# Performance work log

Hardware: AMD Instinct MI355X
Metric: run time of the kernel (lower is better)

The kernel has to match this reference:

```python
import jax, jax.numpy as jnp
import numpy as np

B, T, HID = 2, 2048, 2048
N_HEADS, N_KV, HEAD_DIM = 32, 8, 64
THETA = 10000.0
SCALE = HEAD_DIM ** -0.5
STEPS = 2  # entries already in cache before this call (step_idx)


def _rope_cos_sin(pos):
    # pos: [B, T] int -> cos/sin [B, T, HEAD_DIM]
    inv_freq = 1.0 / (THETA ** (jnp.arange(0, HEAD_DIM, 2, dtype=jnp.float32) / HEAD_DIM))
    freqs = pos.astype(jnp.float32)[..., None] * inv_freq  # [B,T,D/2]
    emb = jnp.concatenate([freqs, freqs], axis=-1)
    return jnp.cos(emb), jnp.sin(emb)


def _rotate_half(x):
    x1, x2 = jnp.split(x, 2, axis=-1)
    return jnp.concatenate([-x2, x1], axis=-1)


def setup_inputs() -> dict:
    key = jax.random.key(0)
    ks = jax.random.split(key, 8)
    combined_states = jax.random.normal(ks[0], (B, T, 2 * HID), dtype=jnp.float32)
    # additive causal mask: 0 on/below diagonal, large negative above
    causal = jnp.tril(jnp.ones((T, T), dtype=bool))
    attention_mask = jnp.where(causal, 0.0, -1e9).astype(jnp.float32)[None, None].repeat(B, axis=0)
    position_ids = jnp.broadcast_to(jnp.arange(T, dtype=jnp.int32), (B, T))
    prev_k = jax.random.normal(ks[1], (STEPS, B, N_HEADS, T, HEAD_DIM), dtype=jnp.float32)
    prev_v = jax.random.normal(ks[2], (STEPS, B, N_HEADS, T, HEAD_DIM), dtype=jnp.float32)
    Wq = 0.02 * jax.random.normal(ks[3], (2 * HID, N_HEADS * HEAD_DIM), dtype=jnp.float32)
    Wk = 0.02 * jax.random.normal(ks[4], (2 * HID, N_KV * HEAD_DIM), dtype=jnp.float32)
    Wv = 0.02 * jax.random.normal(ks[5], (2 * HID, N_KV * HEAD_DIM), dtype=jnp.float32)
    Wo = 0.02 * jax.random.normal(ks[6], (N_HEADS * HEAD_DIM, HID), dtype=jnp.float32)
    return {"combined_states": combined_states, "attention_mask": attention_mask,
            "position_ids": position_ids, "prev_k": prev_k, "prev_v": prev_v,
            "Wq": Wq, "Wk": Wk, "Wv": Wv, "Wo": Wo}


def reference(combined_states, attention_mask, position_ids, prev_k, prev_v, Wq, Wk, Wv, Wo):
    b, t, _ = combined_states.shape
    step_idx = prev_k.shape[0]  # len(cache_k) before append
    groups = N_HEADS // N_KV

    # fused QKV projection -> [B, H, T, D]
    q = (combined_states @ Wq).reshape(b, t, N_HEADS, HEAD_DIM).transpose(0, 2, 1, 3)
    k = (combined_states @ Wk).reshape(b, t, N_KV, HEAD_DIM).transpose(0, 2, 1, 3)
    v = (combined_states @ Wv).reshape(b, t, N_KV, HEAD_DIM).transpose(0, 2, 1, 3)

    # RoPE with phase shift by step_idx
    cos, sin = _rope_cos_sin(position_ids + step_idx)
    cos, sin = cos[:, None], sin[:, None]  # [B,1,T,D]
    q = q * cos + _rotate_half(q) * sin
    k = k * cos + _rotate_half(k) * sin

    # GQA expansion (repeat_interleave over head dim)
    k = jnp.repeat(k, groups, axis=1)
    v = jnp.repeat(v, groups, axis=1)

    # cache after append: [prev_0, prev_1, ..., k_new]; k0 = cache[0], later = cache[1:]
    k0, v0 = prev_k[0], prev_v[0]
    later_k = jnp.concatenate([prev_k[1:], k[None]], axis=0)  # [S, B, H, T, D], S = step_idx
    later_v = jnp.concatenate([prev_v[1:], v[None]], axis=0)

    # block attention over K_0 plus growing diagonal terms
    attn = jnp.einsum('bhtd,bhsd->bhts', q, k0) * SCALE + attention_mask  # [B,H,T,T]
    diag = jnp.einsum('bhtd,sbhtd->bhts', q, later_k) * SCALE             # [B,H,T,S]
    logits = jnp.concatenate([attn, diag], axis=-1)                        # [B,H,T,T+S]
    probs = jax.nn.softmax(logits.astype(jnp.float32), axis=-1).astype(q.dtype)

    out = jnp.einsum('bhts,bhsd->bhtd', probs[..., :t], v0)
    out = out + jnp.einsum('bhts,sbhtd->bhtd', probs[..., t:], later_v)
    out = out.transpose(0, 2, 1, 3).reshape(b, t, N_HEADS * HEAD_DIM)
    return out @ Wo
```

## Files before the change

### kernel.cpp

```cpp
#include <hip/hip_runtime.h>

#define B_    2
#define T_    2048
#define HID_  2048
#define NH_   32
#define NKV_  8
#define HD_   64
#define STEPS_ 2
#define SCALE_ 0.125f
#define CSC_  0.18033688011112042f

typedef float   f32x4  __attribute__((ext_vector_type(4)));
typedef __bf16  bf16x8 __attribute__((ext_vector_type(8)));
typedef unsigned short u16x8 __attribute__((ext_vector_type(8)));

__device__ __forceinline__ unsigned short f2bf(float f) {
  unsigned int u = __builtin_bit_cast(unsigned int, f);
  u = (u + 0x7fffu + ((u >> 16) & 1u)) >> 16;
  return (unsigned short)u;
}
__device__ __forceinline__ float bf2f(unsigned short h) {
  unsigned int u = ((unsigned int)h) << 16;
  return __builtin_bit_cast(float, u);
}
__device__ __forceinline__ bf16x8 frag_ld(const unsigned short* p) {
  u16x8 v = *(const u16x8*)p;
  return __builtin_bit_cast(bf16x8, v);
}
__device__ __forceinline__ f32x4 mfma16(bf16x8 a, bf16x8 b, f32x4 c) {
  return __builtin_amdgcn_mfma_f32_16x16x32_bf16(a, b, c, 0, 0, 0);
}
__device__ __forceinline__ void async_cp16(const void* g, void* l) {
  __builtin_amdgcn_global_load_lds(
      (const __attribute__((address_space(1))) void*)g,
      (__attribute__((address_space(3))) void*)l, 16, 0, 0);
}
__device__ __forceinline__ unsigned int cvtpk_bf16(float lo, float hi) {
  unsigned int r;
  asm("v_cvt_pk_bf16_f32 %0, %1, %2" : "=v"(r) : "v"(lo), "v"(hi));
  return r;
}

__global__ __launch_bounds__(256) void convert_bf16(const float* __restrict__ in,
                                                    unsigned short* __restrict__ out,
                                                    int n4) {
  int idx = blockIdx.x * 256 + threadIdx.x;
  if (idx < n4) {
    float4 v = ((const float4*)in)[idx];
    ushort4 o;
    o.x = f2bf(v.x); o.y = f2bf(v.y); o.z = f2bf(v.z); o.w = f2bf(v.w);
    ((ushort4*)out)[idx] = o;
  }
}

__global__ __launch_bounds__(256) void transpose_f32_bf16_ld(const float* __restrict__ in,
                                                             unsigned short* __restrict__ out,
                                                             int K, int N, int ldo) {
  __shared__ float tile[64][65];
  int n0 = blockIdx.x * 64, k0 = blockIdx.y * 64;
  int c = threadIdx.x & 63, w = threadIdx.x >> 6;
#pragma unroll
  for (int i = 0; i < 16; i++) {
    int r = w * 16 + i;
    tile[r][c] = in[(size_t)(k0 + r) * N + n0 + c];
  }
  __syncthreads();
#pragma unroll
  for (int i = 0; i < 16; i++) {
    int rr = w * 16 + i;
    out[(size_t)(n0 + rr) * ldo + k0 + c] = f2bf(tile[c][rr]);
  }
}

__global__ __launch_bounds__(256) void transpose_v0(const float* __restrict__ v0,
                                                    unsigned short* __restrict__ v0t) {
  __shared__ float tile[64][65];
  int s0 = blockIdx.x * 64;
  int bh = blockIdx.y;
  const float* src = v0 + (size_t)bh * T_ * HD_;
  unsigned short* dst = v0t + (size_t)bh * HD_ * T_;
  int c = threadIdx.x & 63, w = threadIdx.x >> 6;
#pragma unroll
  for (int i = 0; i < 16; i++) {
    int r = w * 16 + i;
    tile[r][c] = src[(size_t)(s0 + r) * HD_ + c];
  }
  __syncthreads();
#pragma unroll
  for (int i = 0; i < 16; i++) {
    int rr = w * 16 + i;
    dst[(size_t)rr * T_ + s0 + c] = f2bf(tile[c][rr]);
  }
}

#define SBAR  do { __builtin_amdgcn_sched_barrier(0); __builtin_amdgcn_s_barrier(); \
                   __builtin_amdgcn_sched_barrier(0); } while (0)
#define LGKM0 do { asm volatile("s_waitcnt lgkmcnt(0)" ::: "memory"); \
                   __builtin_amdgcn_sched_barrier(0); } while (0)
#define VM2   do { asm volatile("s_waitcnt vmcnt(2)" ::: "memory"); } while (0)
#define VM0   do { asm volatile("s_waitcnt vmcnt(0)" ::: "memory"); } while (0)

template <int NF>
__global__ __launch_bounds__(512, 2) void gemm128_bt(const unsigned short* __restrict__ A,
                                                     const unsigned short* __restrict__ Bt,
                                                     float* __restrict__ C,
                                                     int M, int N, int K) {
  constexpr int NHF = NF / 2;
  constexpr int BROWS = 128 + NF * 64;
  __shared__ __attribute__((aligned(128))) unsigned short smem[2][BROWS * 64];

  const int tid  = threadIdx.x;
  const int lane = tid & 63;
  const int wid  = tid >> 6;
  const int wr   = wid >> 2;
  const int wc   = wid & 3;
  const int la   = lane & 15;
  const int lq   = lane >> 4;
  const int sw   = la & 7;
  const int m0   = blockIdx.x * 128;
  const int n0   = blockIdx.y * (NF * 64);

  const int sr = lane >> 3;
  const int sl = (lane & 7) ^ sr;

  const unsigned short* gA[2];
  const unsigned short* gB[NHF][2];
#pragma unroll
  for (int is = 0; is < 2; ++is) {
    int r = (wid * 2 + is) * 8 + sr;
    gA[is] = A + (size_t)(m0 + r) * K + sl * 8;
#pragma unroll
    for (int u = 0; u < NHF; ++u)
      gB[u][is] = Bt + (size_t)(n0 + u * 128 + r) * K + sl * 8;
  }

#define G_STG_A(buf, kt) do { \
    async_cp16(gA[0] + (size_t)(kt) * 64, &smem[buf][(wid * 2 + 0) * 512]); \
    async_cp16(gA[1] + (size_t)(kt) * 64, &smem[buf][(wid * 2 + 1) * 512]); \
  } while (0)
#define G_STG_B(buf, u, kt) do { \
    async_cp16(gB[u][0] + (size_t)(kt) * 64, &smem[buf][(128 + (u) * 128) * 64 + (wid * 2 + 0) * 512]); \
    async_cp16(gB[u][1] + (size_t)(kt) * 64, &smem[buf][(128 + (u) * 128) * 64 + (wid * 2 + 1) * 512]); \
  } while (0)

  f32x4  acc[4][NF] = {};
  bf16x8 aR[2][2], b0r[NHF][2], b1r[NHF][2];

#define G_RD_A(buf, qm) do { \
    const unsigned short* rp_ = &smem[buf][0]; \
    _Pragma("unroll") \
    for (int i_ = 0; i_ < 2; ++i_) { \
      int ro_ = (wr * 64 + (qm) * 32 + i_ * 16 + la) * 64; \
      aR[i_][0] = frag_ld(rp_ + ro_ + (((0 + lq) ^ sw) << 3)); \
      aR[i_][1] = frag_ld(rp_ + ro_ + (((4 + lq) ^ sw) << 3)); \
    } \
  } while (0)
#define G_RD_B(buf, qn, breg) do { \
    const unsigned short* rp_ = &smem[buf][128 * 64]; \
    _Pragma("unroll") \
    for (int j_ = 0; j_ < NHF; ++j_) { \
      int ro_ = (wc * (NF * 16) + (qn) * (NF * 8) + j_ * 16 + la) * 64; \
      breg[j_][0] = frag_ld(rp_ + ro_ + (((0 + lq) ^ sw) << 3)); \
      breg[j_][1] = frag_ld(rp_ + ro_ + (((4 + lq) ^ sw) << 3)); \
    } \
  } while (0)
#define G_MMA(qm, qn, breg) do { \
    _Pragma("unroll") \
    for (int i_ = 0; i_ < 2; ++i_) \
      _Pragma("unroll") \
      for (int j_ = 0; j_ < NHF; ++j_) { \
        f32x4 c_ = acc[(qm) * 2 + i_][(qn) * NHF + j_]; \
        c_ = mfma16(aR[i_][0], breg[j_][0], c_); \
        c_ = mfma16(aR[i_][1], breg[j_][1], c_); \
        acc[(qm) * 2 + i_][(qn) * NHF + j_] = c_; \
      } \
  } while (0)

  G_STG_A(0, 0);
#pragma unroll
  for (int u = 0; u < NHF; ++u) G_STG_B(0, u, 0);
  if constexpr (NF == 6) G_STG_B(1, 2, 1); else G_STG_A(1, 1);
  VM2;
  SBAR;

  const int NI = K >> 7;
  for (int it = 0; it < NI; ++it) {
    const int e = it * 2;
    const bool pf = (it + 1 < NI);
    G_RD_A(0, 0);
    G_RD_B(0, 0, b0r);
    if constexpr (NF == 6) G_STG_A(1, e + 1); else G_STG_B(1, 0, e + 1);
    SBAR; LGKM0;
    __builtin_amdgcn_s_setprio(1); G_MMA(0, 0, b0r); __builtin_amdgcn_s_setprio(0);
    SBAR;
    G_RD_B(0, 1, b1r);
    if constexpr (NF == 6) G_STG_B(1, 0, e + 1); else G_STG_B(1, 1, e + 1);
    SBAR; LGKM0;
    __builtin_amdgcn_s_setprio(1); G_MMA(0, 1, b1r); __builtin_amdgcn_s_setprio(0);
    SBAR;
    G_RD_A(0, 1);
    if constexpr (NF == 6) G_STG_B(1, 1, e + 1);
    SBAR; LGKM0;
    __builtin_amdgcn_s_setprio(1); G_MMA(1, 1, b1r); __builtin_amdgcn_s_setprio(0);
    SBAR;
    if (pf) G_STG_A(0, e + 2);
    SBAR; LGKM0;
    __builtin_amdgcn_s_setprio(1); G_MMA(1, 0, b0r); __builtin_amdgcn_s_setprio(0);
    if (pf) { VM2; } else { VM0; }
    SBAR;
    G_RD_A(1, 0);
    G_RD_B(1, 0, b0r);
    if (pf) G_STG_B(0, 0, e + 2);
    SBAR; LGKM0;
    __builtin_amdgcn_s_setprio(1); G_MMA(0, 0, b0r); __builtin_amdgcn_s_setprio(0);
    SBAR;
    G_RD_B(1, 1, b1r);
    if (pf) G_STG_B(0, 1, e + 2);
    SBAR; LGKM0;
    __builtin_amdgcn_s_setprio(1); G_MMA(0, 1, b1r); __builtin_amdgcn_s_setprio(0);
    SBAR;
    G_RD_A(1, 1);
    if constexpr (NF == 6) { if (pf) G_STG_B(0, 2, e + 2); }
    SBAR; LGKM0;
    __builtin_amdgcn_s_setprio(1); G_MMA(1, 1, b1r); __builtin_amdgcn_s_setprio(0);
    SBAR;
    if constexpr (NF == 6) { if (pf) G_STG_B(1, 2, e + 3); }
    else                   { if (pf) G_STG_A(1, e + 3); }
    SBAR; LGKM0;
    __builtin_amdgcn_s_setprio(1); G_MMA(1, 0, b0r); __builtin_amdgcn_s_setprio(0);
    VM2;
    SBAR;
  }

#pragma unroll
  for (int mf = 0; mf < 4; ++mf) {
    int row = m0 + wr * 64 + mf * 16 + lq * 4;
#pragma unroll
    for (int nf = 0; nf < NF; ++nf) {
      int col = n0 + wc * (NF * 16) + nf * 16 + la;
#pragma unroll
      for (int r = 0; r < 4; ++r)
        C[(size_t)(row + r) * N + col] = acc[mf][nf][r];
    }
  }
#undef G_STG_A
#undef G_STG_B
#undef G_RD_A
#undef G_RD_B
#undef G_MMA
}

__global__ __launch_bounds__(256) void rope_kernel(const float* __restrict__ QKV,
                                                   const int* __restrict__ pos_ids,
                                                   unsigned short* __restrict__ q_b,
                                                   float* __restrict__ knew) {
  int idx = blockIdx.x * 256 + threadIdx.x;
  const int total = B_ * T_ * (NH_ + NKV_) * 32;
  if (idx >= total) return;
  int i = idx & 31;
  int tmp = idx >> 5;
  int hh = tmp % (NH_ + NKV_);
  int bt = tmp / (NH_ + NKV_);
  int t = bt & (T_ - 1);
  int b = bt >> 11;
  int pos = pos_ids[bt] + STEPS_;
  float inv = exp2f(-(float)i * (13.287712379549449f / 32.0f));
  float ang = (float)pos * inv;
  float sn, cs;
  sincosf(ang, &sn, &cs);
  const float* rowp = QKV + (size_t)bt * 3072;
  if (hh < NH_) {
    float x1 = rowp[hh * 64 + i];
    float x2 = rowp[hh * 64 + 32 + i];
    float y1 = (x1 * cs - x2 * sn) * CSC_;
    float y2 = (x2 * cs + x1 * sn) * CSC_;
    size_t o = ((size_t)(b * NH_ + hh) * T_ + t) * HD_ + i;
    q_b[o] = f2bf(y1);
    q_b[o + 32] = f2bf(y2);
  } else {
    int kv = hh - NH_;
    float x1 = rowp[2048 + kv * 64 + i];
    float x2 = rowp[2048 + kv * 64 + 32 + i];
    float y1 = x1 * cs - x2 * sn;
    float y2 = x2 * cs + x1 * sn;
    size_t o = ((size_t)(b * NKV_ + kv) * T_ + t) * HD_ + i;
    knew[o] = y1;
    knew[o + 32] = y2;
  }
}

__global__ __launch_bounds__(256, 3) void flash_kernel(const unsigned short* __restrict__ qb,
                                                       const unsigned short* __restrict__ k0b,
                                                       const unsigned short* __restrict__ v0t,
                                                       float* __restrict__ Of,
                                                       float* __restrict__ ml) {
  __shared__ unsigned short sK[2][64 * 64];
  __shared__ unsigned short sV[2][64 * 64];
  __shared__ unsigned short sP[4][16 * 72];

  const int tid = threadIdx.x;
  const int lane = tid & 63;
  const int wave = tid >> 6;
  const int la = lane & 15;
  const int lq = lane >> 4;
  const int swz = la & 7;

  const int id = blockIdx.x;
  const int bh = (id & 7) * 8 + ((id >> 3) & 7);
  const int qt = 15 - (id >> 6);

  const size_t bhs = (size_t)bh;
  const unsigned short* gK = k0b + bhs * T_ * HD_;
  const unsigned short* gV = v0t + bhs * HD_ * T_;

  const int rb0 = qt * 128 + wave * 32;
  const int ktd = rb0 >> 6;
  const int ktmax = 2 * qt + 1;

  bf16x8 aq[2][2];
#pragma unroll
  for (int f = 0; f < 2; f++) {
    const unsigned short* qp = qb + (bhs * T_ + rb0 + f * 16 + la) * HD_;
    aq[f][0] = frag_ld(qp + lq * 8);
    aq[f][1] = frag_ld(qp + 32 + lq * 8);
  }

  f32x4 o[2][4] = {};
  float m_f[2] = {-1e30f, -1e30f};
  float l_f[2] = {0.0f, 0.0f};

  const int lrow = lane >> 3;
  const int lcb = (lane & 7) ^ lrow;

  {
    unsigned short* kd = &sK[0][wave * 1024];
    unsigned short* vd = &sV[0][wave * 1024];
    async_cp16(gK + (size_t)(wave * 16 + lrow) * HD_ + lcb * 8, kd);
    async_cp16(gK + (size_t)(wave * 16 + 8 + lrow) * HD_ + lcb * 8, kd + 512);
    async_cp16(gV + (size_t)(wave * 16 + lrow) * T_ + lcb * 8, vd);
    async_cp16(gV + (size_t)(wave * 16 + 8 + lrow) * T_ + lcb * 8, vd + 512);
  }
  __syncthreads();

  int cur = 0;
  for (int kt = 0; kt <= ktmax; ++kt) {
    if (kt < ktmax) {
      const int nk = (kt + 1) * 64;
      unsigned short* kd = &sK[cur ^ 1][wave * 1024];
      unsigned short* vd = &sV[cur ^ 1][wave * 1024];
      async_cp16(gK + (size_t)(nk + wave * 16 + lrow) * HD_ + lcb * 8, kd);
      async_cp16(gK + (size_t)(nk + wave * 16 + 8 + lrow) * HD_ + lcb * 8, kd + 512);
      async_cp16(gV + (size_t)(wave * 16 + lrow) * T_ + nk + lcb * 8, vd);
      async_cp16(gV + (size_t)(wave * 16 + 8 + lrow) * T_ + nk + lcb * 8, vd + 512);
    }

    if (kt <= ktd) {
      const unsigned short* kb = &sK[cur][0];
      const unsigned short* vb = &sV[cur][0];

      bf16x8 bk0[4], bk1[4];
#pragma unroll
      for (int nb = 0; nb < 4; nb++) {
        const unsigned short* rp = kb + (nb * 16 + la) * 64;
        bk0[nb] = frag_ld(rp + ((lq ^ swz) << 3));
        bk1[nb] = frag_ld(rp + (((lq + 4) ^ swz) << 3));
      }
      f32x4 s[2][4];
      __builtin_amdgcn_s_setprio(1);
#pragma unroll
      for (int f = 0; f < 2; f++)
#pragma unroll
        for (int nb = 0; nb < 4; nb++) {
          f32x4 z = {0.f, 0.f, 0.f, 0.f};
          z = mfma16(bk0[nb], aq[f][0], z);
          z = mfma16(bk1[nb], aq[f][1], z);
          s[f][nb] = z;
        }
      __builtin_amdgcn_s_setprio(0);

      const bool diag = (kt == ktd);
#pragma unroll
      for (int f = 0; f < 2; f++) {
        const int qrow = rb0 + f * 16 + la;
        if (diag) {
#pragma unroll
          for (int nb = 0; nb < 4; nb++)
#pragma unroll
            for (int r = 0; r < 4; r++) {
              int key = kt * 64 + nb * 16 + lq * 4 + r;
              s[f][nb][r] = (key <= qrow) ? s[f][nb][r] : -1e30f;
            }
        }
        float t0 = fmaxf(fmaxf(s[f][0][0], s[f][0][1]), fmaxf(s[f][0][2], s[f][0][3]));
        float t1 = fmaxf(fmaxf(s[f][1][0], s[f][1][1]), fmaxf(s[f][1][2], s[f][1][3]));
        float t2 = fmaxf(fmaxf(s[f][2][0], s[f][2][1]), fmaxf(s[f][2][2], s[f][2][3]));
        float t3 = fmaxf(fmaxf(s[f][3][0], s[f][3][1]), fmaxf(s[f][3][2], s[f][3][3]));
        float tm = fmaxf(fmaxf(t0, t1), fmaxf(t2, t3));
        tm = fmaxf(tm, __shfl_xor(tm, 16));
        tm = fmaxf(tm, __shfl_xor(tm, 32));
        const bool resc = __any(tm > m_f[f] + 8.0f);
        if (resc) {
          float mn = fmaxf(m_f[f], tm);
          float al = exp2f(m_f[f] - mn);
          m_f[f] = mn;
          l_f[f] *= al;
          float a0 = __shfl(al, lq * 4 + 0);
          float a1 = __shfl(al, lq * 4 + 1);
          float a2 = __shfl(al, lq * 4 + 2);
          float a3 = __shfl(al, lq * 4 + 3);
#pragma unroll
          for (int jd = 0; jd < 4; jd++) {
            o[f][jd][0] *= a0;
            o[f][jd][1] *= a1;
            o[f][jd][2] *= a2;
            o[f][jd][3] *= a3;
          }
        }
        float ls = 0.0f;
#pragma unroll
        for (int nb = 0; nb < 4; nb++)
#pragma unroll
          for (int r = 0; r < 4; r++) {
            float p = exp2f(s[f][nb][r] - m_f[f]);
            s[f][nb][r] = p;
            ls += p;
          }
        ls += __shfl_xor(ls, 16);
        ls += __shfl_xor(ls, 32);
        l_f[f] += ls;
      }

      bf16x8 bv0[4], bv1[4];
#pragma unroll
      for (int jd = 0; jd < 4; jd++) {
        const unsigned short* rp = vb + (jd * 16 + la) * 64;
        bv0[jd] = frag_ld(rp + ((lq ^ swz) << 3));
        bv1[jd] = frag_ld(rp + (((lq + 4) ^ swz) << 3));
      }
      unsigned short* pw = &sP[wave][0];
#pragma unroll
      for (int f = 0; f < 2; f++) {
#pragma unroll
        for (int nb = 0; nb < 4; nb++) {
          unsigned int p01 = cvtpk_bf16(s[f][nb][0], s[f][nb][1]);
          unsigned int p23 = cvtpk_bf16(s[f][nb][2], s[f][nb][3]);
          unsigned long long pq = ((unsigned long long)p23 << 32) | (unsigned long long)p01;
          *(unsigned long long*)(pw + la * 72 + nb * 16 + lq * 4) = pq;
        }
        bf16x8 ap0 = frag_ld(&pw[la * 72 + lq * 8]);
        bf16x8 ap1 = frag_ld(&pw[la * 72 + 32 + lq * 8]);
        __builtin_amdgcn_s_setprio(1);
#pragma unroll
        for (int jd = 0; jd < 4; jd++) {
          o[f][jd] = mfma16(ap0, bv0[jd], o[f][jd]);
          o[f][jd] = mfma16(ap1, bv1[jd], o[f][jd]);
        }
        __builtin_amdgcn_s_setprio(0);
      }
    }
    __syncthreads();
    cur ^= 1;
  }

#pragma unroll
  for (int f = 0; f < 2; f++)
#pragma unroll
    for (int jd = 0; jd < 4; jd++)
#pragma unroll
      for (int r = 0; r < 4; r++) {
        int row = rb0 + f * 16 + lq * 4 + r;
        Of[(bhs * T_ + row) * HD_ + jd * 16 + la] = o[f][jd][r];
      }
  if (lq == 0) {
#pragma unroll
    for (int f = 0; f < 2; f++) {
      int row = rb0 + f * 16 + la;
      ml[(bhs * T_ + row) * 2] = m_f[f];
      ml[(bhs * T_ + row) * 2 + 1] = l_f[f];
    }
  }
}

__global__ __launch_bounds__(256) void attn_epilogue(const unsigned short* __restrict__ qb,
                                                     const float* __restrict__ prev_k,
                                                     const float* __restrict__ prev_v,
                                                     const float* __restrict__ knew,
                                                     const float* __restrict__ QKV,
                                                     const float* __restrict__ Of,
                                                     const float* __restrict__ ml,
                                                     unsigned short* __restrict__ attnout) {
  const int lane = threadIdx.x & 63;
  const int wave = threadIdx.x >> 6;
  const int row = blockIdx.x * 4 + wave;
  const int b = row >> 16;
  const int h = (row >> 11) & 31;
  const int t = row & 2047;
  const int d = lane;
  const size_t base = (size_t)row * HD_ + d;

  float q = bf2f(qb[base]);
  const size_t p1i = ((size_t)B_ * NH_ * T_ * HD_) + (((size_t)b * NH_ + h) * T_ + t) * HD_ + d;
  float k1 = prev_k[p1i];
  float v1 = prev_v[p1i];
  int kv = h >> 2;
  float kn = knew[(((size_t)b * NKV_ + kv) * T_ + t) * HD_ + d];
  float vn = QKV[((size_t)(b * T_ + t)) * 3072 + 2560 + kv * 64 + d];

  float e1 = q * k1, e2 = q * kn;
#pragma unroll
  for (int off = 1; off < 64; off <<= 1) {
    e1 += __shfl_xor(e1, off);
    e2 += __shfl_xor(e2, off);
  }

  float m = ml[(size_t)row * 2];
  float l = ml[(size_t)row * 2 + 1];
  float mf = fmaxf(m, fmaxf(e1, e2));
  float w0 = exp2f(m - mf), w1 = exp2f(e1 - mf), w2 = exp2f(e2 - mf);
  float denom = l * w0 + w1 + w2;
  float out = (Of[base] * w0 + v1 * w1 + vn * w2) / denom;

  attnout[((size_t)(b * T_ + t)) * (NH_ * HD_) + h * HD_ + d] = f2bf(out);
}

#define OFF_QKV   ((size_t)0)
#define OFF_XB    ((size_t)50331648)
#define OFF_WQKVT ((size_t)83886080)
#define OFF_WOT   ((size_t)109051904)
#define OFF_QB    ((size_t)117440512)
#define OFF_K0B   ((size_t)134217728)
#define OFF_V0T   ((size_t)150994944)
#define OFF_KNEW  ((size_t)167772160)
#define OFF_ML    ((size_t)176160768)

extern "C" void kernel_launch(void* const* d_in, const int* in_sizes, int n_in,
                              void* d_out, int out_size, void* d_ws, size_t ws_size,
                              hipStream_t stream) {
  const float* X = (const float*)d_in[0];
  const int* pos = (const int*)d_in[2];
  const float* prevk = (const float*)d_in[3];
  const float* prevv = (const float*)d_in[4];
  const float* Wq = (const float*)d_in[5];
  const float* Wk = (const float*)d_in[6];
  const float* Wv = (const float*)d_in[7];
  const float* Wo = (const float*)d_in[8];

  char* ws = (char*)d_ws;
  float* QKV = (float*)(ws + OFF_QKV);
  unsigned short* Xb = (unsigned short*)(ws + OFF_XB);
  float* Of = (float*)(ws + OFF_XB);
  unsigned short* WqkvT = (unsigned short*)(ws + OFF_WQKVT);
  unsigned short* attnout = (unsigned short*)(ws + OFF_WQKVT);
  unsigned short* WoT = (unsigned short*)(ws + OFF_WOT);
  unsigned short* q_b = (unsigned short*)(ws + OFF_QB);
  unsigned short* k0b = (unsigned short*)(ws + OFF_K0B);
  unsigned short* v0t = (unsigned short*)(ws + OFF_V0T);
  float* knew = (float*)(ws + OFF_KNEW);
  float* ml = (float*)(ws + OFF_ML);

  convert_bf16<<<16384, 256, 0, stream>>>(X, Xb, 4194304);
  transpose_f32_bf16_ld<<<dim3(32, 64), 256, 0, stream>>>(Wq, WqkvT, 4096, 2048, 4096);
  transpose_f32_bf16_ld<<<dim3(8, 64), 256, 0, stream>>>(Wk, WqkvT + (size_t)2048 * 4096, 4096, 512, 4096);
  transpose_f32_bf16_ld<<<dim3(8, 64), 256, 0, stream>>>(Wv, WqkvT + (size_t)2560 * 4096, 4096, 512, 4096);
  transpose_f32_bf16_ld<<<dim3(32, 32), 256, 0, stream>>>(Wo, WoT, 2048, 2048, 2048);
  convert_bf16<<<8192, 256, 0, stream>>>(prevk, k0b, 2097152);
  transpose_v0<<<dim3(32, 64), 256, 0, stream>>>(prevv, v0t);

  gemm128_bt<6><<<dim3(32, 8), 512, 0, stream>>>(Xb, WqkvT, QKV, 4096, 3072, 4096);

  rope_kernel<<<20480, 256, 0, stream>>>(QKV, pos, q_b, knew);

  flash_kernel<<<1024, 256, 0, stream>>>(q_b, k0b, v0t, Of, ml);

  attn_epilogue<<<32768, 256, 0, stream>>>(q_b, prevk, prevv, knew, QKV, Of, ml, attnout);

  gemm128_bt<4><<<dim3(32, 8), 512, 0, stream>>>(attnout, WoT, (float*)d_out, 4096, 2048, 2048);
}
```

Measured before the change: 523.1 us.

## Fuse diagonal-term epilogue into flash attention kernel, drop O/ml round trip

The separate attention epilogue kernel is removed and its work moves into the end of the flash kernel. Each block now computes the two extra diagonal logits from its register-resident Q fragments and combines them with its running max and sum. It then writes the normalized bf16 output directly. This removes the fp32 O and m/l intermediate writes and reads plus one kernel launch, but the fused tail does strided, poorly coalesced global loads of prev_k/prev_v/knew/QKV inside a kernel with occupancy pressure.

```diff
diff --git a/kernel.cpp b/kernel.cpp
--- a/kernel.cpp
+++ b/kernel.cpp
@@ -292,8 +292,11 @@
 __global__ __launch_bounds__(256, 3) void flash_kernel(const unsigned short* __restrict__ qb,
                                                        const unsigned short* __restrict__ k0b,
                                                        const unsigned short* __restrict__ v0t,
-                                                       float* __restrict__ Of,
-                                                       float* __restrict__ ml) {
+                                                       const float* __restrict__ prev_k,
+                                                       const float* __restrict__ prev_v,
+                                                       const float* __restrict__ knew,
+                                                       const float* __restrict__ QKV,
+                                                       unsigned short* __restrict__ attnout) {
   __shared__ unsigned short sK[2][64 * 64];
   __shared__ unsigned short sV[2][64 * 64];
   __shared__ unsigned short sP[4][16 * 72];
@@ -462,65 +465,61 @@
     cur ^= 1;
   }
 
-#pragma unroll
-  for (int f = 0; f < 2; f++)
-#pragma unroll
-    for (int jd = 0; jd < 4; jd++)
-#pragma unroll
-      for (int r = 0; r < 4; r++) {
-        int row = rb0 + f * 16 + lq * 4 + r;
-        Of[(bhs * T_ + row) * HD_ + jd * 16 + la] = o[f][jd][r];
+  const int bI = bh >> 5;
+  const int hI = bh & 31;
+  const int kvI = hI >> 2;
+  const size_t P1 = (size_t)B_ * NH_ * T_ * HD_;
+  const float* k1base = prev_k + P1 + bhs * T_ * HD_;
+  const float* v1base = prev_v + P1 + bhs * T_ * HD_;
+  const float* knbase = knew + ((size_t)bI * NKV_ + kvI) * T_ * HD_;
+  const float* vnbase = QKV + (size_t)bI * T_ * 3072 + 2560 + kvI * 64;
+  unsigned short* aobase = attnout + (size_t)bI * T_ * (NH_ * HD_) + hI * HD_;
+
+#pragma unroll
+  for (int f = 0; f < 2; f++) {
+    const int rowA = rb0 + f * 16 + la;
+    const float* k1p = k1base + (size_t)rowA * HD_;
+    const float* knp = knbase + (size_t)rowA * HD_;
+    float e1 = 0.f, e2 = 0.f;
+#pragma unroll
+    for (int h2 = 0; h2 < 2; h2++) {
+      const int dd = h2 * 32 + lq * 8;
+#pragma unroll
+      for (int j = 0; j < 8; j++) {
+        float qv = (float)aq[f][h2][j];
+        e1 = fmaf(qv, k1p[dd + j], e1);
+        e2 = fmaf(qv, knp[dd + j], e2);
       }
-  if (lq == 0) {
-#pragma unroll
-    for (int f = 0; f < 2; f++) {
-      int row = rb0 + f * 16 + la;
-      ml[(bhs * T_ + row) * 2] = m_f[f];
-      ml[(bhs * T_ + row) * 2 + 1] = l_f[f];
     }
-  }
-}
-
-__global__ __launch_bounds__(256) void attn_epilogue(const unsigned short* __restrict__ qb,
-                                                     const float* __restrict__ prev_k,
-                                                     const float* __restrict__ prev_v,
-                                                     const float* __restrict__ knew,
-                                                     const float* __restrict__ QKV,
-                                                     const float* __restrict__ Of,
-                                                     const float* __restrict__ ml,
-                                                     unsigned short* __restrict__ attnout) {
-  const int lane = threadIdx.x & 63;
-  const int wave = threadIdx.x >> 6;
-  const int row = blockIdx.x * 4 + wave;
-  const int b = row >> 16;
-  const int h = (row >> 11) & 31;
-  const int t = row & 2047;
-  const int d = lane;
-  const size_t base = (size_t)row * HD_ + d;
-
-  float q = bf2f(qb[base]);
-  const size_t p1i = ((size_t)B_ * NH_ * T_ * HD_) + (((size_t)b * NH_ + h) * T_ + t) * HD_ + d;
-  float k1 = prev_k[p1i];
-  float v1 = prev_v[p1i];
-  int kv = h >> 2;
-  float kn = knew[(((size_t)b * NKV_ + kv) * T_ + t) * HD_ + d];
-  float vn = QKV[((size_t)(b * T_ + t)) * 3072 + 2560 + kv * 64 + d];
-
-  float e1 = q * k1, e2 = q * kn;
-#pragma unroll
-  for (int off = 1; off < 64; off <<= 1) {
-    e1 += __shfl_xor(e1, off);
-    e2 += __shfl_xor(e2, off);
-  }
-
-  float m = ml[(size_t)row * 2];
-  float l = ml[(size_t)row * 2 + 1];
-  float mf = fmaxf(m, fmaxf(e1, e2));
-  float w0 = exp2f(m - mf), w1 = exp2f(e1 - mf), w2 = exp2f(e2 - mf);
-  float denom = l * w0 + w1 + w2;
-  float out = (Of[base] * w0 + v1 * w1 + vn * w2) / denom;
-
-  attnout[((size_t)(b * T_ + t)) * (NH_ * HD_) + h * HD_ + d] = f2bf(out);
+    e1 += __shfl_xor(e1, 16); e1 += __shfl_xor(e1, 32);
+    e2 += __shfl_xor(e2, 16); e2 += __shfl_xor(e2, 32);
+    float mx = fmaxf(m_f[f], fmaxf(e1, e2));
+    float w0 = exp2f(m_f[f] - mx);
+    float w1 = exp2f(e1 - mx);
+    float w2 = exp2f(e2 - mx);
+    float inv = 1.0f / (l_f[f] * w0 + w1 + w2);
+    float s0 = w0 * inv, s1 = w1 * inv, s2 = w2 * inv;
+    float a0[4], a1[4], a2[4];
+#pragma unroll
+    for (int r = 0; r < 4; r++) {
+      a0[r] = __shfl(s0, lq * 4 + r);
+      a1[r] = __shfl(s1, lq * 4 + r);
+      a2[r] = __shfl(s2, lq * 4 + r);
+    }
+#pragma unroll
+    for (int r = 0; r < 4; r++) {
+      const int rowO = rb0 + f * 16 + lq * 4 + r;
+      const float* v1p = v1base + (size_t)rowO * HD_;
+      const float* vnp = vnbase + (size_t)rowO * 3072;
+      unsigned short* aop = aobase + (size_t)rowO * (NH_ * HD_);
+#pragma unroll
+      for (int jd = 0; jd < 4; jd++) {
+        int d = jd * 16 + la;
+        float out = o[f][jd][r] * a0[r] + v1p[d] * a1[r] + vnp[d] * a2[r];
+        aop[d] = f2bf(out);
+      }
+    }
+  }
 }
 
 #define OFF_QKV   ((size_t)0)
@@ -548,7 +547,6 @@
   char* ws = (char*)d_ws;
   float* QKV = (float*)(ws + OFF_QKV);
   unsigned short* Xb = (unsigned short*)(ws + OFF_XB);
-  float* Of = (float*)(ws + OFF_XB);
   unsigned short* WqkvT = (unsigned short*)(ws + OFF_WQKVT);
   unsigned short* attnout = (unsigned short*)(ws + OFF_WQKVT);
   unsigned short* WoT = (unsigned short*)(ws + OFF_WOT);
@@ -556,7 +554,6 @@
   unsigned short* k0b = (unsigned short*)(ws + OFF_K0B);
   unsigned short* v0t = (unsigned short*)(ws + OFF_V0T);
   float* knew = (float*)(ws + OFF_KNEW);
-  float* ml = (float*)(ws + OFF_ML);
 
   convert_bf16<<<16384, 256, 0, stream>>>(X, Xb, 4194304);
   transpose_f32_bf16_ld<<<dim3(32, 64), 256, 0, stream>>>(Wq, WqkvT, 4096, 2048, 4096);
@@ -570,9 +567,7 @@
 
   rope_kernel<<<20480, 256, 0, stream>>>(QKV, pos, q_b, knew);
 
-  flash_kernel<<<1024, 256, 0, stream>>>(q_b, k0b, v0t, Of, ml);
-
-  attn_epilogue<<<32768, 256, 0, stream>>>(q_b, prevk, prevv, knew, QKV, Of, ml, attnout);
+  flash_kernel<<<1024, 256, 0, stream>>>(q_b, k0b, v0t, prevk, prevv, knew, QKV, attnout);
 
   gemm128_bt<4><<<dim3(32, 8), 512, 0, stream>>>(attnout, WoT, (float*)d_out, 4096, 2048, 2048);
 }
```

Result: no change. 518.0 us (-1.0%).
